# Kernel tuning notes

Measured on AMD Instinct MI355X. Metric: run time of the kernel, lower is better.

The kernel has to match this reference:

```python
import jax, jax.numpy as jnp
import numpy as np

N_ANCHORS = 250000
IMG_H, IMG_W = 1024, 1024
PRE_NMS = 6000    # num_pre_nms_test (inference path, training=False)
POST_NMS = 300    # num_post_nms_test
IOU_THR = 0.7


def setup_inputs() -> dict:
    key = jax.random.key(0)
    k1, k2, k3, k4, k5 = jax.random.split(key, 5)
    bboxes_txtytwth = jax.random.normal(k1, (N_ANCHORS, 4), dtype=jnp.float32) * 0.1
    # anchors as (ymin, xmin, ymax, xmax) scattered over the image
    cy = jax.random.uniform(k2, (N_ANCHORS,), dtype=jnp.float32) * IMG_H
    cx = jax.random.uniform(k3, (N_ANCHORS,), dtype=jnp.float32) * IMG_W
    ah = 32.0 + jax.random.uniform(k4, (N_ANCHORS,), dtype=jnp.float32) * 224.0
    aw = 32.0 + jax.random.uniform(k5, (N_ANCHORS,), dtype=jnp.float32) * 224.0
    anchors = jnp.stack([cy - 0.5 * ah, cx - 0.5 * aw,
                         cy + 0.5 * ah, cx + 0.5 * aw], axis=1)
    scores = jax.random.normal(jax.random.fold_in(key, 7), (N_ANCHORS,), dtype=jnp.float32)
    return {
        "bboxes_txtytwth": bboxes_txtytwth,
        "anchors": anchors,
        "scores": scores,
        "image_height": IMG_H,
        "image_width": IMG_W,
        "extractor_stride": 16,
    }


def _decode_bbox(anchors, deltas):
    # anchors: [N,4] (ymin,xmin,ymax,xmax); deltas: [N,4] (ty,tx,th,tw)
    h = anchors[:, 2] - anchors[:, 0]
    w = anchors[:, 3] - anchors[:, 1]
    cy = anchors[:, 0] + 0.5 * h
    cx = anchors[:, 1] + 0.5 * w
    ty, tx, th, tw = deltas[:, 0], deltas[:, 1], deltas[:, 2], deltas[:, 3]
    ncy = ty * h + cy
    ncx = tx * w + cx
    nh = jnp.exp(th) * h
    nw = jnp.exp(tw) * w
    return jnp.stack([ncy - 0.5 * nh, ncx - 0.5 * nw,
                      ncy + 0.5 * nh, ncx + 0.5 * nw], axis=1)


def _iou_matrix(b):
    # b: [K,4] -> [K,K] pairwise IoU
    area = (b[:, 2] - b[:, 0]) * (b[:, 3] - b[:, 1])
    iy = jnp.maximum(0.0, jnp.minimum(b[:, None, 2], b[None, :, 2]) -
                     jnp.maximum(b[:, None, 0], b[None, :, 0]))
    ix = jnp.maximum(0.0, jnp.minimum(b[:, None, 3], b[None, :, 3]) -
                     jnp.maximum(b[:, None, 1], b[None, :, 1]))
    inter = iy * ix
    return inter / (area[:, None] + area[None, :] - inter + 1e-9)


def _rpn_proposal(bboxes_txtytwth, anchors, scores, image_height, image_width,
                  extractor_stride):
    # 1) decode
    boxes = _decode_bbox(anchors, bboxes_txtytwth)
    # 2) clip to image + min-edge filter (filter implemented as score mask)
    ymin = jnp.clip(boxes[:, 0], 0.0, image_height)
    xmin = jnp.clip(boxes[:, 1], 0.0, image_width)
    ymax = jnp.clip(boxes[:, 2], 0.0, image_height)
    xmax = jnp.clip(boxes[:, 3], 0.0, image_width)
    boxes = jnp.stack([ymin, xmin, ymax, xmax], axis=1)
    valid = ((ymax - ymin) >= extractor_stride) & ((xmax - xmin) >= extractor_stride)
    masked_scores = jnp.where(valid, scores, -jnp.inf)
    # 3) pre-NMS top-k (sorted descending by score)
    top_scores, top_idx = jax.lax.top_k(masked_scores, PRE_NMS)
    top_boxes = boxes[top_idx]                      # [PRE_NMS,4]
    valid_k = jnp.isfinite(top_scores)
    # 4) greedy NMS over score-sorted boxes
    iou = _iou_matrix(top_boxes)                    # [PRE_NMS, PRE_NMS]
    order = jnp.arange(PRE_NMS)

    def body(i, suppressed):
        alive_i = jnp.logical_not(suppressed[i]) & valid_k[i]
        return suppressed | (alive_i & (iou[i] > IOU_THR) & (order > i))

    suppressed = jax.lax.fori_loop(0, PRE_NMS, body,
                                   jnp.zeros((PRE_NMS,), dtype=bool))
    keep = jnp.logical_not(suppressed) & valid_k
    # 5) first POST_NMS kept boxes (already score-ordered), fixed-shape output
    rank = jnp.cumsum(keep) - 1                     # position among kept
    tgt = jnp.where(keep & (rank < POST_NMS), rank, POST_NMS)
    out = jnp.zeros((POST_NMS + 1, 4), dtype=top_boxes.dtype).at[tgt].set(top_boxes)
    return out[:POST_NMS]                           # [POST_NMS,4], zero-padded


def reference(bboxes_txtytwth, anchors, scores, image_height, image_width,
              extractor_stride):
    return _rpn_proposal(bboxes_txtytwth, anchors, scores,
                         float(image_height), float(image_width),
                         float(extractor_stride))
```

## Files before the change

kernel.cpp:

```cpp
#include <hip/hip_runtime.h>

#pragma clang fp contract(off)

#define N_PRE   6000
#define N_POST  300
#define NW      94
#define SELCAP  7936
#define RS_BLK  124
#define NBIN    16384
#define DSHIFT  18
#define HPART   64

struct SelState {
    unsigned int thr;
};

__global__ void decode_kernel(const float4* __restrict__ deltas,
                              const float4* __restrict__ anchors,
                              const float*  __restrict__ scores,
                              const int* __restrict__ ph, const int* __restrict__ pw,
                              const int* __restrict__ ps,
                              unsigned int* __restrict__ s32out,
                              float4* __restrict__ boxes,
                              unsigned long long* __restrict__ sel,
                              unsigned long long* __restrict__ valid_words,
                              unsigned int* __restrict__ counter, int N)
{
#pragma clang fp contract(off)
    if (blockIdx.x == 0) {
        for (int t = threadIdx.x; t < SELCAP; t += 256) sel[t] = 0ull;
    } else if (blockIdx.x == 1) {
        if (threadIdx.x < 128) valid_words[threadIdx.x] = 0ull;
        if (threadIdx.x == 0) *counter = 0u;
    }
    int i = blockIdx.x * blockDim.x + threadIdx.x;
    if (i >= N) return;
    float H = (float)(*ph), W = (float)(*pw), S = (float)(*ps);
    float4 d = deltas[i];
    float4 a = anchors[i];
    float h = a.z - a.x, w = a.w - a.y;
    float cy = a.x + 0.5f * h, cx = a.y + 0.5f * w;
    float ncy = d.x * h + cy;
    float ncx = d.y * w + cx;
    float eh = (float)exp((double)d.z);
    float ew = (float)exp((double)d.w);
    float nh = eh * h;
    float nw = ew * w;
    float ymin = ncy - 0.5f * nh, xmin = ncx - 0.5f * nw;
    float ymax = ncy + 0.5f * nh, xmax = ncx + 0.5f * nw;
    ymin = fminf(fmaxf(ymin, 0.0f), H);
    xmin = fminf(fmaxf(xmin, 0.0f), W);
    ymax = fminf(fmaxf(ymax, 0.0f), H);
    xmax = fminf(fmaxf(xmax, 0.0f), W);
    bool valid = (ymax - ymin >= S) && (xmax - xmin >= S);
    float sc = scores[i];
    unsigned int bits = __float_as_uint(sc);
    unsigned int s32;
    if (!valid) s32 = 0x007FFFFFu;
    else        s32 = (bits & 0x80000000u) ? ~bits : (bits | 0x80000000u);
    s32out[i] = s32;
    boxes[i]  = make_float4(ymin, xmin, ymax, xmax);
}

__global__ __launch_bounds__(256) void hist_part(const unsigned int* __restrict__ s32in,
                                                 unsigned int* __restrict__ phist, int N)
{
    __shared__ unsigned int lh[NBIN];
    int tid = threadIdx.x;
    for (int j = tid; j < NBIN; j += 256) lh[j] = 0u;
    __syncthreads();
    for (int i = blockIdx.x * 256 + tid; i < N; i += HPART * 256)
        atomicAdd(&lh[s32in[i] >> DSHIFT], 1u);
    __syncthreads();
    unsigned int* dst = phist + blockIdx.x * NBIN;
    for (int j = tid; j < NBIN; j += 256) dst[j] = lh[j];
}

__global__ __launch_bounds__(256) void hist_reduce(const unsigned int* __restrict__ phist,
                                                   unsigned int* __restrict__ hist)
{
    int j = blockIdx.x * 256 + threadIdx.x;
    unsigned int s = 0;
#pragma unroll 8
    for (int b = 0; b < HPART; b++) s += phist[b * NBIN + j];
    hist[j] = s;
}

__global__ __launch_bounds__(1024) void pick_pass(const unsigned int* __restrict__ hist,
                                                  SelState* __restrict__ state)
{
    __shared__ unsigned int wsum[16];
    __shared__ int sel_chunk;
    __shared__ unsigned int sel_above;
    int tid = threadIdx.x, lane = tid & 63, wave = tid >> 6;
    const unsigned int k = 6000u;

    unsigned int s = 0;
    int base = tid * 16;
#pragma unroll
    for (int i = 0; i < 16; i++) s += hist[base + i];
    unsigned int S = s;
    for (int d = 1; d < 64; d <<= 1) {
        unsigned int t = __shfl_down(S, d);
        if (lane + d < 64) S += t;
    }
    if (lane == 0) wsum[wave] = S;
    __syncthreads();
    unsigned int above = 0;
    for (int w2 = wave + 1; w2 < 16; w2++) above += wsum[w2];
    unsigned int F  = S + above;
    unsigned int Fn = F - s;
    if (Fn < k && k <= F) { sel_chunk = tid; sel_above = Fn; }
    __syncthreads();
    int c = sel_chunk;
    unsigned int acc = sel_above;
    if (wave == 0 && lane < 16) {
        unsigned int b = hist[c * 16 + lane];
        unsigned int B = b;
        for (int d = 1; d < 16; d <<= 1) {
            unsigned int t = __shfl_down(B, d);
            if (lane + d < 16) B += t;
        }
        unsigned int Bn = B - b;
        unsigned int kk = k - acc;
        if (Bn < kk && kk <= B) state->thr = (unsigned int)(c * 16 + lane);
    }
}

__global__ void compact_kernel(const unsigned int* __restrict__ s32in,
                               const SelState* __restrict__ state,
                               unsigned long long* __restrict__ sel,
                               unsigned int* __restrict__ counter, int N)
{
    int i = blockIdx.x * blockDim.x + threadIdx.x;
    if (i >= N) return;
    unsigned int s32 = s32in[i];
    if ((s32 >> DSHIFT) >= state->thr) {
        unsigned int p = atomicAdd(counter, 1u);
        if (p < SELCAP)
            sel[p] = ((unsigned long long)s32 << 32) |
                     (unsigned long long)(~(unsigned int)i);
    }
}

__global__ __launch_bounds__(256) void rank_scatter(
    const unsigned long long* __restrict__ sel,
    const float4* __restrict__ boxes,
    float4* __restrict__ boxes_sorted,
    unsigned long long* __restrict__ valid_words, int N)
{
    __shared__ __align__(16) unsigned long long kbuf[SELCAP];
    __shared__ unsigned int cnt4[4][64];
    int tid = threadIdx.x;
    for (int t = tid; t < SELCAP; t += 256) kbuf[t] = sel[t];
    __syncthreads();
    int lane = tid & 63;
    int slice = tid >> 6;
    int i = blockIdx.x * 64 + lane;
    unsigned long long my = kbuf[i];
    const int SL = SELCAP / 4;
    int j0 = slice * SL;
    unsigned int c = 0;
#pragma unroll 8
    for (int j = j0; j < j0 + SL; j += 2) {
        ulonglong2 kk = *reinterpret_cast<const ulonglong2*>(&kbuf[j]);
        c += (kk.x > my) || (kk.x == my && j < i);
        c += (kk.y > my) || (kk.y == my && (j + 1) < i);
    }
    cnt4[slice][lane] = c;
    __syncthreads();
    if (tid < 64) {
        unsigned int rank = cnt4[0][tid] + cnt4[1][tid] + cnt4[2][tid] + cnt4[3][tid];
        unsigned long long key = kbuf[blockIdx.x * 64 + tid];
        if (key != 0ull && rank < N_PRE) {
            unsigned int s32 = (unsigned int)(key >> 32);
            unsigned int ii  = ~(unsigned int)(key & 0xFFFFFFFFull);
            float4 b = (ii < (unsigned int)N) ? boxes[ii] : make_float4(0.f,0.f,0.f,0.f);
            boxes_sorted[rank] = b;
            bool v = (s32 != 0x007FFFFFu) && (ii < (unsigned int)N);
            if (v) atomicOr(&valid_words[rank >> 6], 1ull << (rank & 63));
        }
    }
}

__global__ __launch_bounds__(64) void mask_kernel(const float4* __restrict__ boxes_sorted,
                                                  unsigned long long* __restrict__ mask)
{
#pragma clang fp contract(off)
    int rb = blockIdx.y, cb = blockIdx.x;
    if (cb < rb) return;
    __shared__ float4 cbox[64];
    int tid = threadIdx.x;
    int col0 = cb * 64;
    int c = col0 + tid;
    cbox[tid] = (c < N_PRE) ? boxes_sorted[c] : make_float4(0.f, 0.f, 0.f, 0.f);
    __syncthreads();
    int i = rb * 64 + tid;
    if (i >= N_PRE) return;
    float4 bi = boxes_sorted[i];
    float area_i = (bi.z - bi.x) * (bi.w - bi.y);
    unsigned long long word = 0ull;
#pragma unroll 8
    for (int j = 0; j < 64; j++) {
        float4 bj = cbox[j];
        float iy = fminf(bi.z, bj.z) - fmaxf(bi.x, bj.x);
        iy = fmaxf(iy, 0.0f);
        float ix = fminf(bi.w, bj.w) - fmaxf(bi.y, bj.y);
        ix = fmaxf(ix, 0.0f);
        float inter = iy * ix;
        float area_j = (bj.z - bj.x) * (bj.w - bj.y);
        float iou = inter / (((area_i + area_j) - inter) + 1e-9f);
        if ((col0 + j) > i && iou > 0.7f) word |= (1ull << j);
    }
    mask[(size_t)i * NW + cb] = word;
}

__global__ __launch_bounds__(64) void nms_seq(const unsigned long long* __restrict__ mask,
                                              const unsigned long long* __restrict__ valid_words,
                                              const float4* __restrict__ boxes_sorted,
                                              float* __restrict__ out)
{
#pragma clang fp contract(off)
    int lane = threadIdx.x;
    float4* out4 = reinterpret_cast<float4*>(out);

    for (int t = lane; t < N_POST; t += 64)
        out4[t] = make_float4(0.f, 0.f, 0.f, 0.f);

    unsigned long long vw0 = valid_words[lane];
    unsigned long long vw1 = (lane < NW - 64) ? valid_words[64 + lane] : 0ull;

    int s0 = -1, s1 = -1, s2 = -1, s3 = -1, s4 = -1;

    int rank = 0;
    float4 cb = boxes_sorted[lane];
    for (int w = 0; w < NW; w++) {
        float4 nb;
        if (w < NW - 1) nb = boxes_sorted[(w + 1) * 64 + lane];

        unsigned long long m0 = 0, m1 = 0, m2 = 0, m3 = 0, m4 = 0;
        if (s0 >= 0) m0 = mask[(size_t)s0 * NW + w];
        if (s1 >= 0) m1 = mask[(size_t)s1 * NW + w];
        if (s2 >= 0) m2 = mask[(size_t)s2 * NW + w];
        if (s3 >= 0) m3 = mask[(size_t)s3 * NW + w];
        if (s4 >= 0) m4 = mask[(size_t)s4 * NW + w];
        unsigned long long m = (m0 | m1) | (m2 | m3) | m4;
        for (int d = 1; d < 64; d <<= 1) m |= __shfl_xor(m, d);

        unsigned long long vw = (w < 64) ? __shfl(vw0, w) : __shfl(vw1, w - 64);
        unsigned long long aw = vw & ~m;

        if (aw) {
            float area_me = (cb.z - cb.x) * (cb.w - cb.y);
            while (aw) {
                int b = __builtin_ctzll(aw);
                float kx = __shfl(cb.x, b);
                float ky = __shfl(cb.y, b);
                float kz = __shfl(cb.z, b);
                float kw = __shfl(cb.w, b);
                float iy = fmaxf(fminf(cb.z, kz) - fmaxf(cb.x, kx), 0.0f);
                float ix = fmaxf(fminf(cb.w, kw) - fmaxf(cb.y, ky), 0.0f);
                float inter = iy * ix;
                float ka = (kz - kx) * (kw - ky);
                float iou = inter / (((area_me + ka) - inter) + 1e-9f);
                unsigned long long sup = __ballot(iou > 0.7f);
                if (lane == b) out4[rank] = cb;
                int idx = w * 64 + b;
                if ((rank & 63) == lane) {
                    switch (rank >> 6) {
                        case 0: s0 = idx; break;
                        case 1: s1 = idx; break;
                        case 2: s2 = idx; break;
                        case 3: s3 = idx; break;
                        default: s4 = idx; break;
                    }
                }
                rank++;
                if (rank >= N_POST) break;
                aw &= ~(sup | (1ull << b));
            }
        }
        if (rank >= N_POST) break;
        cb = nb;
    }
}

extern "C" void kernel_launch(void* const* d_in, const int* in_sizes, int n_in,
                              void* d_out, int out_size, void* d_ws, size_t ws_size,
                              hipStream_t stream)
{
    const float4* deltas  = (const float4*)d_in[0];
    const float4* anchors = (const float4*)d_in[1];
    const float*  scores  = (const float*)d_in[2];
    const int* ph = (const int*)d_in[3];
    const int* pw = (const int*)d_in[4];
    const int* ps = (const int*)d_in[5];
    int N = in_sizes[2];

    char* base = (char*)d_ws;
    size_t off = 0;
    auto alloc = [&](size_t sz) -> void* {
        void* p = base + off;
        off = (off + sz + 255) & ~(size_t)255;
        return p;
    };
    unsigned int* s32buf = (unsigned int*)alloc(sizeof(unsigned int) * (size_t)N);
    float4* boxes = (float4*)alloc(sizeof(float4) * (size_t)N);
    unsigned int* phist = (unsigned int*)alloc((size_t)HPART * NBIN * sizeof(unsigned int));
    unsigned int* hist = (unsigned int*)alloc(NBIN * sizeof(unsigned int));
    SelState* state = (SelState*)alloc(256);
    unsigned int* counter = (unsigned int*)alloc(256);
    unsigned long long* valid_words = (unsigned long long*)alloc(128 * 8);
    unsigned long long* sel = (unsigned long long*)alloc(sizeof(unsigned long long) * SELCAP);
    float4* boxes_sorted = (float4*)alloc(sizeof(float4) * 6016);
    unsigned long long* mask = (unsigned long long*)alloc(sizeof(unsigned long long) * (size_t)N_PRE * NW);

    int nb = (N + 255) / 256;
    decode_kernel<<<nb, 256, 0, stream>>>(deltas, anchors, scores, ph, pw, ps,
                                          s32buf, boxes, sel, valid_words, counter, N);
    hist_part<<<HPART, 256, 0, stream>>>(s32buf, phist, N);
    hist_reduce<<<NBIN / 256, 256, 0, stream>>>(phist, hist);
    pick_pass<<<1, 1024, 0, stream>>>(hist, state);
    compact_kernel<<<nb, 256, 0, stream>>>(s32buf, state, sel, counter, N);
    rank_scatter<<<RS_BLK, 256, 0, stream>>>(sel, boxes, boxes_sorted, valid_words, N);
    mask_kernel<<<dim3(NW, NW), 64, 0, stream>>>(boxes_sorted, mask);
    nms_seq<<<1, 64, 0, stream>>>(mask, valid_words, boxes_sorted, (float*)d_out);
}
```

Measured before the change: 300.1 us.

## Restructure sequential NMS to accumulate removed bits and pipeline mask row loads

```diff
diff --git a/kernel.cpp b/kernel.cpp
--- a/kernel.cpp
+++ b/kernel.cpp
@@ -229,60 +229,81 @@
 
     unsigned long long vw0 = valid_words[lane];
     unsigned long long vw1 = (lane < NW - 64) ? valid_words[64 + lane] : 0ull;
-
-    int s0 = -1, s1 = -1, s2 = -1, s3 = -1, s4 = -1;
-
+    unsigned long long rem0 = ~vw0;
+    unsigned long long rem1 = ~vw1;
+
+    unsigned long long pA_lo[8] = {0,0,0,0,0,0,0,0}, pA_hi[8] = {0,0,0,0,0,0,0,0};
+    unsigned long long pB_lo[8] = {0,0,0,0,0,0,0,0}, pB_hi[8] = {0,0,0,0,0,0,0,0};
+
+    unsigned long long carry = 0ull;
     int rank = 0;
+
+    int row0 = lane;
+    unsigned long long dg_d = mask[(size_t)row0 * NW + 0];
+    unsigned long long dg_b = mask[(size_t)row0 * NW + 1];
     float4 cb = boxes_sorted[lane];
-    for (int w = 0; w < NW; w++) {
-        float4 nb;
-        if (w < NW - 1) nb = boxes_sorted[(w + 1) * 64 + lane];
-
-        unsigned long long m0 = 0, m1 = 0, m2 = 0, m3 = 0, m4 = 0;
-        if (s0 >= 0) m0 = mask[(size_t)s0 * NW + w];
-        if (s1 >= 0) m1 = mask[(size_t)s1 * NW + w];
-        if (s2 >= 0) m2 = mask[(size_t)s2 * NW + w];
-        if (s3 >= 0) m3 = mask[(size_t)s3 * NW + w];
-        if (s4 >= 0) m4 = mask[(size_t)s4 * NW + w];
-        unsigned long long m = (m0 | m1) | (m2 | m3) | m4;
-        for (int d = 1; d < 64; d <<= 1) m |= __shfl_xor(m, d);
-
-        unsigned long long vw = (w < 64) ? __shfl(vw0, w) : __shfl(vw1, w - 64);
-        unsigned long long aw = vw & ~m;
-
-        if (aw) {
-            float area_me = (cb.z - cb.x) * (cb.w - cb.y);
-            while (aw) {
-                int b = __builtin_ctzll(aw);
-                float kx = __shfl(cb.x, b);
-                float ky = __shfl(cb.y, b);
-                float kz = __shfl(cb.z, b);
-                float kw = __shfl(cb.w, b);
-                float iy = fmaxf(fminf(cb.z, kz) - fmaxf(cb.x, kx), 0.0f);
-                float ix = fmaxf(fminf(cb.w, kw) - fmaxf(cb.y, ky), 0.0f);
-                float inter = iy * ix;
-                float ka = (kz - kx) * (kw - ky);
-                float iou = inter / (((area_me + ka) - inter) + 1e-9f);
-                unsigned long long sup = __ballot(iou > 0.7f);
-                if (lane == b) out4[rank] = cb;
-                int idx = w * 64 + b;
-                if ((rank & 63) == lane) {
-                    switch (rank >> 6) {
-                        case 0: s0 = idx; break;
-                        case 1: s1 = idx; break;
-                        case 2: s2 = idx; break;
-                        case 3: s3 = idx; break;
-                        default: s4 = idx; break;
-                    }
-                }
-                rank++;
-                if (rank >= N_POST) break;
-                aw &= ~(sup | (1ull << b));
-            }
-        }
-        if (rank >= N_POST) break;
-        cb = nb;
-    }
+
+#define WORD_STEP(WV, PLO, PHI)                                                 \
+    {                                                                           \
+        int w = (WV);                                                           \
+               \
+        rem0 |= ((PLO[0]|PLO[1])|(PLO[2]|PLO[3]))|((PLO[4]|PLO[5])|(PLO[6]|PLO[7])); \
+        rem1 |= ((PHI[0]|PHI[1])|(PHI[2]|PHI[3]))|((PHI[4]|PHI[5])|(PHI[6]|PHI[7])); \
+             \
+        unsigned long long dgn_d = 0ull, dgn_b = 0ull;                          \
+        float4 cbn = cb;                                                        \
+        if (w + 1 < NW) {                                                       \
+            int rown = (w + 1) * 64 + lane;                                     \
+            if (rown > N_PRE - 1) rown = N_PRE - 1;                             \
+            dgn_d = mask[(size_t)rown * NW + (w + 1)];                          \
+            dgn_b = mask[(size_t)rown * NW + (w + 2)];                          \
+            cbn = boxes_sorted[(w + 1) * 64 + lane];                            \
+        }                                                                       \
+        unsigned long long remw = (w < 64) ? __shfl(rem0, w) : __shfl(rem1, w - 64); \
+        unsigned long long vw   = (w < 64) ? __shfl(vw0, w)  : __shfl(vw1, w - 64); \
+        unsigned long long alive = vw & ~remw & ~carry;                         \
+        carry = 0ull;                                                           \
+        unsigned long long keptb = 0ull;                                        \
+        while (alive) {                                                         \
+            int b = __builtin_ctzll(alive);                   \
+            unsigned long long dxb = __shfl(dg_d, b);                           \
+            unsigned long long dyb = __shfl(dg_b, b);                           \
+            if (lane == b) out4[rank] = cb;                                     \
+            keptb |= 1ull << b;                                                 \
+            rank++;                                                             \
+            if (rank >= N_POST) break;                                          \
+            alive &= ~(dxb | (1ull << b));                                      \
+            carry |= dyb;                                                       \
+        }                                                                       \
+        if (rank >= N_POST) break;                                              \
+                     \
+        {                                                                       \
+            int kc = __popcll(keptb);                                           \
+            unsigned long long kb = keptb;                                      \
+            _Pragma("unroll")                                                   \
+            for (int sslot = 0; sslot < 8; sslot++) {                           \
+                if (sslot < kc) {                                               \
+                    int bb = __builtin_ctzll(kb); kb &= kb - 1ull;              \
+                    const unsigned long long* rp = mask + (size_t)(w * 64 + bb) * NW; \
+                    PLO[sslot] = rp[lane];                                      \
+                    PHI[sslot] = (lane < NW - 64) ? rp[64 + lane] : 0ull;       \
+                } else { PLO[sslot] = 0ull; PHI[sslot] = 0ull; }                \
+            }                                                                   \
+            while (kb) {            \
+                int bb = __builtin_ctzll(kb); kb &= kb - 1ull;                  \
+                const unsigned long long* rp = mask + (size_t)(w * 64 + bb) * NW; \
+                rem0 |= rp[lane];                                               \
+                if (lane < NW - 64) rem1 |= rp[64 + lane];                      \
+            }                                                                   \
+        }                                                                       \
+        dg_d = dgn_d; dg_b = dgn_b; cb = cbn;                                   \
+    }
+
+    for (int w2 = 0; w2 < NW; w2 += 2) {
+        WORD_STEP(w2,     pA_lo, pA_hi)
+        WORD_STEP(w2 + 1, pB_lo, pB_hi)
+    }
+#undef WORD_STEP
 }
 
 extern "C" void kernel_launch(void* const* d_in, const int* in_sizes, int n_in,
@@ -313,7 +334,7 @@
     unsigned long long* valid_words = (unsigned long long*)alloc(128 * 8);
     unsigned long long* sel = (unsigned long long*)alloc(sizeof(unsigned long long) * SELCAP);
     float4* boxes_sorted = (float4*)alloc(sizeof(float4) * 6016);
-    unsigned long long* mask = (unsigned long long*)alloc(sizeof(unsigned long long) * (size_t)N_PRE * NW);
+    unsigned long long* mask = (unsigned long long*)alloc(sizeof(unsigned long long) * ((size_t)N_PRE * NW + 32));
 
     int nb = (N + 255) / 256;
     decode_kernel<<<nb, 256, 0, stream>>>(deltas, anchors, scores, ph, pw, ps,
```

New measurement: 313.3 us. 1.04x slower.

## Pipeline NMS suppression with transposed diagonal masks and async LDS row prefetch

Applied to the files above, without the earlier changes.

```diff
diff --git a/kernel.cpp b/kernel.cpp
--- a/kernel.cpp
+++ b/kernel.cpp
@@ -14,6 +14,19 @@
 struct SelState {
     unsigned int thr;
 };
+
+static __device__ __forceinline__ unsigned long long readlane64(unsigned long long v, int l) {
+    unsigned lo = __builtin_amdgcn_readlane((unsigned)v, l);
+    unsigned hi = __builtin_amdgcn_readlane((unsigned)(v >> 32), l);
+    return ((unsigned long long)hi << 32) | lo;
+}
+
+static __device__ __forceinline__ void gload_lds16(const void* gsrc, void* ldst) {
+    __builtin_amdgcn_global_load_lds(
+        (const __attribute__((address_space(1))) unsigned int*)(uintptr_t)gsrc,
+        (__attribute__((address_space(3))) unsigned int*)(unsigned int)(uintptr_t)ldst,
+        16, 0, 0);
+}
 
 __global__ void decode_kernel(const float4* __restrict__ deltas,
                               const float4* __restrict__ anchors,
@@ -24,14 +37,20 @@
                               float4* __restrict__ boxes,
                               unsigned long long* __restrict__ sel,
                               unsigned long long* __restrict__ valid_words,
-                              unsigned int* __restrict__ counter, int N)
+                              unsigned int* __restrict__ counter,
+                              unsigned long long* __restrict__ dbT4,
+                              unsigned long long* __restrict__ zrow, int N)
 {
 #pragma clang fp contract(off)
     if (blockIdx.x == 0) {
         for (int t = threadIdx.x; t < SELCAP; t += 256) sel[t] = 0ull;
     } else if (blockIdx.x == 1) {
         if (threadIdx.x < 128) valid_words[threadIdx.x] = 0ull;
+        if (threadIdx.x < 128) zrow[threadIdx.x] = 0ull;
         if (threadIdx.x == 0) *counter = 0u;
+    } else if (blockIdx.x >= 2 && blockIdx.x <= 5) {
+        int base = (blockIdx.x - 2) * (NW * 64);
+        for (int t = threadIdx.x; t < NW * 64; t += 256) dbT4[base + t] = 0ull;
     }
     int i = blockIdx.x * blockDim.x + threadIdx.x;
     if (i >= N) return;
@@ -143,22 +162,23 @@
     }
 }
 
-__global__ __launch_bounds__(256) void rank_scatter(
+__global__ __launch_bounds__(1024) void rank_scatter(
     const unsigned long long* __restrict__ sel,
     const float4* __restrict__ boxes,
     float4* __restrict__ boxes_sorted,
     unsigned long long* __restrict__ valid_words, int N)
 {
     __shared__ __align__(16) unsigned long long kbuf[SELCAP];
-    __shared__ unsigned int cnt4[4][64];
+    __shared__ unsigned int cnt[64];
     int tid = threadIdx.x;
-    for (int t = tid; t < SELCAP; t += 256) kbuf[t] = sel[t];
+    if (tid < 64) cnt[tid] = 0u;
+    for (int t = tid; t < SELCAP; t += 1024) kbuf[t] = sel[t];
     __syncthreads();
     int lane = tid & 63;
     int slice = tid >> 6;
     int i = blockIdx.x * 64 + lane;
     unsigned long long my = kbuf[i];
-    const int SL = SELCAP / 4;
+    const int SL = SELCAP / 16;
     int j0 = slice * SL;
     unsigned int c = 0;
 #pragma unroll 8
@@ -167,10 +187,10 @@
         c += (kk.x > my) || (kk.x == my && j < i);
         c += (kk.y > my) || (kk.y == my && (j + 1) < i);
     }
-    cnt4[slice][lane] = c;
+    atomicAdd(&cnt[lane], c);
     __syncthreads();
     if (tid < 64) {
-        unsigned int rank = cnt4[0][tid] + cnt4[1][tid] + cnt4[2][tid] + cnt4[3][tid];
+        unsigned int rank = cnt[tid];
         unsigned long long key = kbuf[blockIdx.x * 64 + tid];
         if (key != 0ull && rank < N_PRE) {
             unsigned int s32 = (unsigned int)(key >> 32);
@@ -184,7 +204,8 @@
 }
 
 __global__ __launch_bounds__(64) void mask_kernel(const float4* __restrict__ boxes_sorted,
-                                                  unsigned long long* __restrict__ mask)
+                                                  unsigned long long* __restrict__ mask,
+                                                  unsigned long long* __restrict__ dbT4)
 {
 #pragma clang fp contract(off)
     int rb = blockIdx.y, cb = blockIdx.x;
@@ -213,14 +234,28 @@
         if ((col0 + j) > i && iou > 0.7f) word |= (1ull << j);
     }
     mask[(size_t)i * NW + cb] = word;
-}
-
-__global__ __launch_bounds__(64) void nms_seq(const unsigned long long* __restrict__ mask,
-                                              const unsigned long long* __restrict__ valid_words,
-                                              const float4* __restrict__ boxes_sorted,
-                                              float* __restrict__ out)
+
+    int dd = cb - rb;
+    if (dd <= 3) {
+        unsigned long long colw = 0ull;
+        for (int jj = 0; jj < 64; jj++) {
+            unsigned long long t = __ballot((unsigned int)((word >> jj) & 1ull));
+            if (tid == jj) colw = t;
+        }
+        dbT4[(size_t)(rb * 64 + tid) * 4 + dd] = colw;
+    }
+}
+
+__global__ __launch_bounds__(64) void nms_seq(
+    const unsigned long long* __restrict__ mask,
+    const unsigned long long* __restrict__ dbT4,
+    const unsigned long long* __restrict__ valid_words,
+    const unsigned long long* __restrict__ zrow,
+    const float4* __restrict__ boxes_sorted,
+    float* __restrict__ out)
 {
 #pragma clang fp contract(off)
+    __shared__ unsigned long long stag[4][8][128];
     int lane = threadIdx.x;
     float4* out4 = reinterpret_cast<float4*>(out);
 
@@ -229,60 +264,107 @@
 
     unsigned long long vw0 = valid_words[lane];
     unsigned long long vw1 = (lane < NW - 64) ? valid_words[64 + lane] : 0ull;
-
-    int s0 = -1, s1 = -1, s2 = -1, s3 = -1, s4 = -1;
-
+    unsigned long long rem0 = ~vw0;
+    unsigned long long rem1 = ~vw1;
+
+    unsigned long long inc1 = 0ull, inc2 = 0ull, inc3 = 0ull;
+
+    int k0 = -1, k1 = -1, k2 = -1, k3 = -1, k4 = -1;
     int rank = 0;
-    float4 cb = boxes_sorted[lane];
+
+    ulonglong2 dba = *reinterpret_cast<const ulonglong2*>(&dbT4[(size_t)lane * 4]);
+    ulonglong2 dbb = *reinterpret_cast<const ulonglong2*>(&dbT4[(size_t)lane * 4 + 2]);
+    unsigned long long dT = dba.x, bT1 = dba.y, bT2 = dbb.x, bT3 = dbb.y;
+
+#pragma unroll 1
     for (int w = 0; w < NW; w++) {
-        float4 nb;
-        if (w < NW - 1) nb = boxes_sorted[(w + 1) * 64 + lane];
-
-        unsigned long long m0 = 0, m1 = 0, m2 = 0, m3 = 0, m4 = 0;
-        if (s0 >= 0) m0 = mask[(size_t)s0 * NW + w];
-        if (s1 >= 0) m1 = mask[(size_t)s1 * NW + w];
-        if (s2 >= 0) m2 = mask[(size_t)s2 * NW + w];
-        if (s3 >= 0) m3 = mask[(size_t)s3 * NW + w];
-        if (s4 >= 0) m4 = mask[(size_t)s4 * NW + w];
-        unsigned long long m = (m0 | m1) | (m2 | m3) | m4;
-        for (int d = 1; d < 64; d <<= 1) m |= __shfl_xor(m, d);
-
-        unsigned long long vw = (w < 64) ? __shfl(vw0, w) : __shfl(vw1, w - 64);
-        unsigned long long aw = vw & ~m;
-
-        if (aw) {
-            float area_me = (cb.z - cb.x) * (cb.w - cb.y);
-            while (aw) {
-                int b = __builtin_ctzll(aw);
-                float kx = __shfl(cb.x, b);
-                float ky = __shfl(cb.y, b);
-                float kz = __shfl(cb.z, b);
-                float kw = __shfl(cb.w, b);
-                float iy = fmaxf(fminf(cb.z, kz) - fmaxf(cb.x, kx), 0.0f);
-                float ix = fmaxf(fminf(cb.w, kw) - fmaxf(cb.y, ky), 0.0f);
-                float inter = iy * ix;
-                float ka = (kz - kx) * (kw - ky);
-                float iou = inter / (((area_me + ka) - inter) + 1e-9f);
-                unsigned long long sup = __ballot(iou > 0.7f);
-                if (lane == b) out4[rank] = cb;
+        if (w >= 4) {
+            asm volatile("s_waitcnt vmcnt(28)" ::: "memory");
+            __builtin_amdgcn_sched_barrier(0);
+            int g = w & 3;
+#pragma unroll
+            for (int s = 0; s < 8; s++) {
+                rem0 |= stag[g][s][lane];
+                if (lane < NW - 64) rem1 |= stag[g][s][64 + lane];
+            }
+        }
+
+        unsigned long long dTn = 0ull, b1n = 0ull, b2n = 0ull, b3n = 0ull;
+        if (w + 1 < NW) {
+            ulonglong2 na = *reinterpret_cast<const ulonglong2*>(
+                &dbT4[(size_t)((w + 1) * 64 + lane) * 4]);
+            ulonglong2 nb = *reinterpret_cast<const ulonglong2*>(
+                &dbT4[(size_t)((w + 1) * 64 + lane) * 4 + 2]);
+            dTn = na.x; b1n = na.y; b2n = nb.x; b3n = nb.y;
+        }
+
+        unsigned long long remw = (w < 64) ? readlane64(rem0, w)
+                                           : readlane64(rem1, w - 64);
+        unsigned long long vw   = (w < 64) ? readlane64(vw0, w)
+                                           : readlane64(vw1, w - 64);
+        unsigned long long alive = vw & ~remw & ~inc1;
+
+        unsigned int ca1 = 0u, ca2 = 0u, ca3 = 0u;
+        unsigned long long keptb = 0ull;
+        while (alive) {
+            int b = __builtin_ctzll(alive);
+            unsigned int supd = (unsigned int)((dT >> b) & 1ull);
+            ca1 |= (unsigned int)((bT1 >> b) & 1ull);
+            ca2 |= (unsigned int)((bT2 >> b) & 1ull);
+            ca3 |= (unsigned int)((bT3 >> b) & 1ull);
+            keptb |= 1ull << b;
+            if ((rank & 63) == lane) {
                 int idx = w * 64 + b;
-                if ((rank & 63) == lane) {
-                    switch (rank >> 6) {
-                        case 0: s0 = idx; break;
-                        case 1: s1 = idx; break;
-                        case 2: s2 = idx; break;
-                        case 3: s3 = idx; break;
-                        default: s4 = idx; break;
-                    }
+                switch (rank >> 6) {
+                    case 0: k0 = idx; break;
+                    case 1: k1 = idx; break;
+                    case 2: k2 = idx; break;
+                    case 3: k3 = idx; break;
+                    default: k4 = idx; break;
                 }
-                rank++;
-                if (rank >= N_POST) break;
-                aw &= ~(sup | (1ull << b));
             }
+            rank++;
+            if (rank >= N_POST) break;
+            unsigned long long supw = __ballot(supd);
+            alive &= ~(supw | (1ull << b));
         }
         if (rank >= N_POST) break;
-        cb = nb;
-    }
+
+        inc1 = inc2 | __ballot(ca1);
+        inc2 = inc3 | __ballot(ca2);
+        inc3 = __ballot(ca3);
+
+        {
+            int kc = __popcll(keptb);
+            unsigned long long kb = keptb;
+            int g = w & 3;
+#pragma unroll
+            for (int s = 0; s < 8; s++) {
+                const void* src;
+                if (s < kc) {
+                    int bb = __builtin_ctzll(kb); kb &= kb - 1ull;
+                    src = (const char*)(mask + (size_t)(w * 64 + bb) * NW) + lane * 16;
+                } else {
+                    src = (const char*)zrow + lane * 16;
+                }
+                gload_lds16(src, (void*)&stag[g][s][0]);
+            }
+            while (kb) {
+                int bb = __builtin_ctzll(kb); kb &= kb - 1ull;
+                const unsigned long long* rp = mask + (size_t)(w * 64 + bb) * NW;
+                if (lane >= w) rem0 |= rp[lane];
+                if (lane < NW - 64 && 64 + lane >= w) rem1 |= rp[64 + lane];
+            }
+        }
+
+        dT = dTn; bT1 = b1n; bT2 = b2n; bT3 = b3n;
+    }
+
+    if (k0 >= 0) out4[0 * 64 + lane] = boxes_sorted[k0];
+    if (k1 >= 0) out4[1 * 64 + lane] = boxes_sorted[k1];
+    if (k2 >= 0) out4[2 * 64 + lane] = boxes_sorted[k2];
+    if (k3 >= 0) out4[3 * 64 + lane] = boxes_sorted[k3];
+    if (k4 >= 0 && (4 * 64 + lane) < N_POST) out4[4 * 64 + lane] = boxes_sorted[k4];
 }
 
 extern "C" void kernel_launch(void* const* d_in, const int* in_sizes, int n_in,
@@ -311,18 +393,21 @@
     SelState* state = (SelState*)alloc(256);
     unsigned int* counter = (unsigned int*)alloc(256);
     unsigned long long* valid_words = (unsigned long long*)alloc(128 * 8);
+    unsigned long long* zrow = (unsigned long long*)alloc(128 * 8);
     unsigned long long* sel = (unsigned long long*)alloc(sizeof(unsigned long long) * SELCAP);
     float4* boxes_sorted = (float4*)alloc(sizeof(float4) * 6016);
-    unsigned long long* mask = (unsigned long long*)alloc(sizeof(unsigned long long) * (size_t)N_PRE * NW);
+    unsigned long long* dbT4 = (unsigned long long*)alloc(sizeof(unsigned long long) * (size_t)NW * 64 * 4);
+    unsigned long long* mask = (unsigned long long*)alloc(sizeof(unsigned long long) * ((size_t)N_PRE * NW + 64));
 
     int nb = (N + 255) / 256;
     decode_kernel<<<nb, 256, 0, stream>>>(deltas, anchors, scores, ph, pw, ps,
-                                          s32buf, boxes, sel, valid_words, counter, N);
+                                          s32buf, boxes, sel, valid_words, counter,
+                                          dbT4, zrow, N);
     hist_part<<<HPART, 256, 0, stream>>>(s32buf, phist, N);
     hist_reduce<<<NBIN / 256, 256, 0, stream>>>(phist, hist);
     pick_pass<<<1, 1024, 0, stream>>>(hist, state);
     compact_kernel<<<nb, 256, 0, stream>>>(s32buf, state, sel, counter, N);
-    rank_scatter<<<RS_BLK, 256, 0, stream>>>(sel, boxes, boxes_sorted, valid_words, N);
-    mask_kernel<<<dim3(NW, NW), 64, 0, stream>>>(boxes_sorted, mask);
-    nms_seq<<<1, 64, 0, stream>>>(mask, valid_words, boxes_sorted, (float*)d_out);
-}
+    rank_scatter<<<RS_BLK, 1024, 0, stream>>>(sel, boxes, boxes_sorted, valid_words, N);
+    mask_kernel<<<dim3(NW, NW), 64, 0, stream>>>(boxes_sorted, mask, dbT4);
+    nms_seq<<<1, 64, 0, stream>>>(mask, dbT4, valid_words, zrow, boxes_sorted, (float*)d_out);
+}
```

After: 338.6 us. +12.8%, slower.
